# Optimization experiments

Measured on AMD Instinct MI355X. Metric: run time of the kernel, lower is better.

Reference implementation:

```python
import jax, jax.numpy as jnp
import numpy as np

NUM_HEADS = 4
TEMPERATURE = 1.0
EDGE_WEIGHT = 0.5


def setup_inputs() -> dict:
    key = jax.random.key(0)
    k1, k2, k3 = jax.random.split(key, 3)
    x = jax.random.normal(k1, (4, 2048, 512), dtype=jnp.float32)
    gate_w = jax.random.normal(k2, (1, 1), dtype=jnp.float32)
    gate_b = jax.random.normal(k3, (1,), dtype=jnp.float32)
    return {"x": x, "gate_w": gate_w, "gate_b": gate_b}


def _forward(x, gate_w, gate_b):
    B, N, C = x.shape
    H = NUM_HEADS
    hd = C // H
    # F.normalize(x, dim=-1) with eps=1e-12
    norm = jnp.linalg.norm(x, axis=-1, keepdims=True)
    x_norm = x / jnp.maximum(norm, 1e-12)
    # multi-head cosine-sim attention
    xh = x_norm.reshape(B, N, H, hd).transpose(0, 2, 1, 3)  # (B,H,N,hd)
    sim = jnp.einsum("bhnd,bhmd->bhnm", xh, xh) / (hd ** 0.5 * TEMPERATURE)
    attn = jax.nn.softmax(sim, axis=-1)
    xv = x.reshape(B, N, H, hd).transpose(0, 2, 1, 3)  # (B,H,N,hd)
    x_refined = jnp.einsum("bhnm,bhmd->bhnd", attn, xv)
    x_refined = x_refined.transpose(0, 2, 1, 3).reshape(B, N, C)
    # edge-variance mask (no_grad in torch -> stop_gradient)
    diff = jnp.var(x, axis=-1, keepdims=True, ddof=1)  # (B,N,1), unbiased like torch
    edge_mask = jax.nn.sigmoid((diff - diff.mean()) / (jnp.std(diff, ddof=1) + 1e-6))
    edge_mask = jax.lax.stop_gradient(edge_mask)
    x_refined = (1.0 + EDGE_WEIGHT * edge_mask) * x_refined
    # scalar gate: Linear(1,1) + Sigmoid on global mean
    gate_input = x.mean(axis=1, keepdims=True).mean(axis=-1, keepdims=True)  # (B,1,1)
    gate = jax.nn.sigmoid(gate_input * gate_w[0, 0] + gate_b[0])
    x_refined = gate * x_refined
    return x + x_refined


def reference(x, gate_w, gate_b):
    return _forward(x, gate_w, gate_b)
```

## Files before the change

kernel.cpp:

```cpp
#include <hip/hip_runtime.h>
#include <stdint.h>

#define B_   4
#define N_   2048
#define C_   512
#define H_   4
#define HD_  128
#define BN_  (B_ * N_)
#define NIT_ 32
#define SCALE_ 0.08838834764831845f

typedef __attribute__((ext_vector_type(8))) short  short8;
typedef __attribute__((ext_vector_type(4))) unsigned short ushort4_t;
typedef __attribute__((ext_vector_type(4))) float  float4_t;
typedef __attribute__((ext_vector_type(8))) __bf16 bf16x8;

static __device__ __forceinline__ unsigned short f2bf(float f) {
  union { float f; uint32_t u; } v; v.f = f;
  uint32_t r = v.u + 0x7FFFu + ((v.u >> 16) & 1u);
  return (unsigned short)(r >> 16);
}

static __device__ __forceinline__ float4_t mfma16(short8 a, short8 b, float4_t c) {
  return __builtin_amdgcn_mfma_f32_16x16x32_bf16(
      __builtin_bit_cast(bf16x8, a), __builtin_bit_cast(bf16x8, b), c, 0, 0, 0);
}

#define GLOAD16(SRC, DST)                                               \
  __builtin_amdgcn_global_load_lds(                                     \
      (const __attribute__((address_space(1))) void*)(SRC),             \
      (__attribute__((address_space(3))) void*)(DST), 16, 0, 0)

__global__ __launch_bounds__(256) void k_stats(
    const float* __restrict__ x, unsigned short* __restrict__ xnq,
    float* __restrict__ diff, float* __restrict__ toksum) {
  int tok  = blockIdx.x * 4 + (threadIdx.x >> 6);
  int lane = threadIdx.x & 63;
  const float* xr = x + (size_t)tok * C_;
  float4_t a = *(const float4_t*)(xr + lane * 8);
  float4_t b = *(const float4_t*)(xr + lane * 8 + 4);
  float s = 0.f, ss = 0.f;
#pragma unroll
  for (int j = 0; j < 4; ++j) {
    s  += a[j] + b[j];
    ss += a[j] * a[j] + b[j] * b[j];
  }
#pragma unroll
  for (int o = 1; o < 64; o <<= 1) {
    s  += __shfl_xor(s, o);
    ss += __shfl_xor(ss, o);
  }
  float rn = 1.f / fmaxf(sqrtf(ss), 1e-12f);
  short8 o8;
#pragma unroll
  for (int j = 0; j < 4; ++j) {
    o8[j]     = (short)f2bf(a[j] * rn);
    o8[j + 4] = (short)f2bf(b[j] * rn);
  }
  *(short8*)(xnq + (size_t)tok * C_ + lane * 8) = o8;
  if (lane == 0) {
    diff[tok]   = (ss - s * s * (1.f / C_)) * (1.f / (C_ - 1));
    toksum[tok] = s;
  }
}

__global__ __launch_bounds__(256) void k_transpose(
    const float* __restrict__ x, unsigned short* __restrict__ xvT) {
  __shared__ float tr[HD_][65];
  int bh = blockIdx.x & 15, nt = blockIdx.x >> 4;
  int b = bh >> 2, h = bh & 3;
  int n0 = nt * 64, c0 = h * HD_;
  int t = threadIdx.x;
  int dm = (t & 31) * 4;
  int nr = t >> 5;
#pragma unroll
  for (int p = 0; p < 8; ++p) {
    int n = p * 8 + nr;
    float4_t v = *(const float4_t*)(x + ((size_t)(b * N_ + n0 + n)) * C_ + c0 + dm);
#pragma unroll
    for (int k = 0; k < 4; ++k) tr[dm + k][n] = v[k];
  }
  __syncthreads();
#pragma unroll
  for (int p = 0; p < 4; ++p) {
    int c = p * 256 + t;
    int d = c >> 3, nc = (c & 7) * 8;
    short8 o8;
#pragma unroll
    for (int e = 0; e < 8; ++e) o8[e] = (short)f2bf(tr[d][nc + e]);
    *(short8*)(xvT + ((size_t)bh * HD_ + d) * N_ + n0 + nc) = o8;
  }
}

__global__ __launch_bounds__(256) void k_finalize(
    const float* __restrict__ diff, const float* __restrict__ toksum,
    const float* __restrict__ gw, const float* __restrict__ gb,
    float* __restrict__ stats) {
  __shared__ float sh[4][8];
  int t = threadIdx.x, l = t & 63, w = t >> 6;
  float s1 = 0.f, s2 = 0.f;
  for (int i = t; i < BN_; i += 256) { float d = diff[i]; s1 += d; s2 += d * d; }
  float bs0 = 0.f, bs1 = 0.f, bs2 = 0.f, bs3 = 0.f;
  for (int i = t; i < N_; i += 256) {
    bs0 += toksum[i];          bs1 += toksum[N_ + i];
    bs2 += toksum[2 * N_ + i]; bs3 += toksum[3 * N_ + i];
  }
#pragma unroll
  for (int o = 1; o < 64; o <<= 1) {
    s1 += __shfl_xor(s1, o);  s2 += __shfl_xor(s2, o);
    bs0 += __shfl_xor(bs0, o); bs1 += __shfl_xor(bs1, o);
    bs2 += __shfl_xor(bs2, o); bs3 += __shfl_xor(bs3, o);
  }
  if (l == 0) {
    sh[w][0] = s1; sh[w][1] = s2;
    sh[w][2] = bs0; sh[w][3] = bs1; sh[w][4] = bs2; sh[w][5] = bs3;
  }
  __syncthreads();
  if (t == 0) {
    float S1 = sh[0][0] + sh[1][0] + sh[2][0] + sh[3][0];
    float S2 = sh[0][1] + sh[1][1] + sh[2][1] + sh[3][1];
    float mean = S1 / (float)BN_;
    float var  = (S2 - S1 * S1 / (float)BN_) / (float)(BN_ - 1);
    float rstd = 1.f / (sqrtf(var) + 1e-6f);
    stats[0] = mean; stats[1] = rstd;
    float w00 = gw[0], bb = gb[0];
#pragma unroll
    for (int q = 0; q < 4; ++q) {
      float bsum = sh[0][2 + q] + sh[1][2 + q] + sh[2][2 + q] + sh[3][2 + q];
      float gi = bsum / (float)(N_ * C_);
      stats[2 + q] = 1.f / (1.f + __expf(-(gi * w00 + bb)));
    }
  }
}

__global__ __launch_bounds__(128) void k_attn(
    const float* __restrict__ x, const unsigned short* __restrict__ xnq,
    const unsigned short* __restrict__ xvT, const float* __restrict__ diff,
    const float* __restrict__ stats, float* __restrict__ out) {
  __shared__ unsigned short sm[32768];
  int i  = blockIdx.x;
  int bh = ((i & 7) << 1) | ((i >> 3) & 1);
  int qt = i >> 4;
  int b = bh >> 2, h = bh & 3, c0 = h * HD_;
  int tid = threadIdx.x, w = tid >> 6, l = tid & 63;
  int g = l >> 4, r = l & 15;
  int q0 = qt * 64 + w * 32;

  short8 qf[2][4];
  const unsigned short* qbase = xnq + ((size_t)(b * N_ + q0)) * C_ + c0;
#pragma unroll
  for (int sub = 0; sub < 2; ++sub)
#pragma unroll
    for (int cs = 0; cs < 4; ++cs)
      qf[sub][cs] = *(const short8*)(qbase + (size_t)(sub * 16 + r) * C_ + g * 8 + cs * 32);

  float4_t acc[2][8];
  float ls[2] = {0.f, 0.f};
#pragma unroll
  for (int sub = 0; sub < 2; ++sub)
#pragma unroll
    for (int dt = 0; dt < 8; ++dt)
      acc[sub][dt] = (float4_t){0.f, 0.f, 0.f, 0.f};

  auto stage = [&](int it, int cb) {
    const unsigned short* ks = xnq + ((size_t)(b * N_ + it * 64)) * C_ + c0;
    unsigned short* kd = &sm[cb * 8192];
#pragma unroll
    for (int jj = 0; jj < 8; ++jj) {
      int j = w * 8 + jj;
      int row = 4 * j + g;
      int ssl = r ^ (row & 15);
      GLOAD16(ks + (size_t)row * C_ + ssl * 8, kd + j * 512);
    }
    const unsigned short* vs = xvT + ((size_t)bh * HD_) * N_ + it * 64;
    unsigned short* vd = &sm[16384 + cb * 8192];
#pragma unroll
    for (int jj = 0; jj < 8; ++jj) {
      int j = w * 8 + jj;
      int d = 8 * j + (l >> 3);
      int ssl = (l & 7) ^ (d & 7);
      GLOAD16(vs + (size_t)d * N_ + ssl * 8, vd + j * 512);
    }
  };

  stage(0, 0);
  __syncthreads();

  for (int it = 0; it < NIT_; ++it) {
    int cb = it & 1;
    if (it + 1 < NIT_) stage(it + 1, cb ^ 1);
    const unsigned short* K = &sm[cb * 8192];
    const unsigned short* V = &sm[16384 + cb * 8192];

    float4_t p[2][4];
#pragma unroll
    for (int sub = 0; sub < 2; ++sub)
#pragma unroll
      for (int t4 = 0; t4 < 4; ++t4)
        p[sub][t4] = (float4_t){0.f, 0.f, 0.f, 0.f};

#pragma unroll
    for (int t4 = 0; t4 < 4; ++t4) {
#pragma unroll
      for (int cs = 0; cs < 4; ++cs) {
        short8 kf = *(const short8*)(K + (size_t)(t4 * 16 + r) * 128 +
                                     ((g * 8 + cs * 32) ^ (r * 8)));
        p[0][t4] = mfma16(kf, qf[0][cs], p[0][t4]);
        p[1][t4] = mfma16(kf, qf[1][cs], p[1][t4]);
      }
    }

    short8 pf[2][2];
#pragma unroll
    for (int sub = 0; sub < 2; ++sub)
#pragma unroll
      for (int t4 = 0; t4 < 4; ++t4) {
        float e0 = __expf(p[sub][t4][0] * SCALE_);
        float e1 = __expf(p[sub][t4][1] * SCALE_);
        float e2 = __expf(p[sub][t4][2] * SCALE_);
        float e3 = __expf(p[sub][t4][3] * SCALE_);
        ls[sub] += (e0 + e1) + (e2 + e3);
        pf[sub][t4 >> 1][(t4 & 1) * 4 + 0] = (short)f2bf(e0);
        pf[sub][t4 >> 1][(t4 & 1) * 4 + 1] = (short)f2bf(e1);
        pf[sub][t4 >> 1][(t4 & 1) * 4 + 2] = (short)f2bf(e2);
        pf[sub][t4 >> 1][(t4 & 1) * 4 + 3] = (short)f2bf(e3);
      }

    int sw = (r & 7) * 8;
#pragma unroll
    for (int dt = 0; dt < 8; ++dt) {
      const unsigned short* vrow = V + (size_t)(dt * 16 + r) * 64;
      union { short8 s8; ushort4_t h[2]; } vf0, vf1;
      vf0.h[0] = *(const ushort4_t*)(vrow + ((g * 4)      ^ sw));
      vf0.h[1] = *(const ushort4_t*)(vrow + ((g * 4 + 16) ^ sw));
      vf1.h[0] = *(const ushort4_t*)(vrow + ((g * 4 + 32) ^ sw));
      vf1.h[1] = *(const ushort4_t*)(vrow + ((g * 4 + 48) ^ sw));
      acc[0][dt] = mfma16(vf0.s8, pf[0][0], acc[0][dt]);
      acc[0][dt] = mfma16(vf1.s8, pf[0][1], acc[0][dt]);
      acc[1][dt] = mfma16(vf0.s8, pf[1][0], acc[1][dt]);
      acc[1][dt] = mfma16(vf1.s8, pf[1][1], acc[1][dt]);
    }
    __syncthreads();
  }

#pragma unroll
  for (int sub = 0; sub < 2; ++sub) {
    ls[sub] += __shfl_xor(ls[sub], 16);
    ls[sub] += __shfl_xor(ls[sub], 32);
  }
  float mean = stats[0], rstd = stats[1], gate = stats[2 + b];
#pragma unroll
  for (int sub = 0; sub < 2; ++sub) {
    int q = q0 + sub * 16 + r;
    float dv = diff[b * N_ + q];
    float em = 1.f / (1.f + __expf(-(dv - mean) * rstd));
    float f  = gate * (1.f + 0.5f * em) / ls[sub];
    const float* xr = x + ((size_t)(b * N_ + q)) * C_;
    float* orow = out + ((size_t)(b * N_ + q)) * C_;
#pragma unroll
    for (int dt = 0; dt < 8; ++dt) {
      int dcol = c0 + dt * 16 + g * 4;
      float4_t xin = *(const float4_t*)(xr + dcol);
      float4_t o;
#pragma unroll
      for (int j = 0; j < 4; ++j) o[j] = xin[j] + f * acc[sub][dt][j];
      *(float4_t*)(orow + dcol) = o;
    }
  }
}

extern "C" void kernel_launch(void* const* d_in, const int* in_sizes, int n_in,
                              void* d_out, int out_size, void* d_ws, size_t ws_size,
                              hipStream_t stream) {
  (void)in_sizes; (void)n_in; (void)out_size; (void)ws_size;
  const float* x  = (const float*)d_in[0];
  const float* gw = (const float*)d_in[1];
  const float* gb = (const float*)d_in[2];
  float* out = (float*)d_out;
  unsigned short* xnq = (unsigned short*)d_ws;
  unsigned short* xvT = xnq + (size_t)BN_ * C_;
  float* diff   = (float*)(xvT + (size_t)BN_ * C_);
  float* toksum = diff + BN_;
  float* stats  = toksum + BN_;
  hipLaunchKernelGGL(k_stats, dim3(BN_ / 4), dim3(256), 0, stream, x, xnq, diff, toksum);
  hipLaunchKernelGGL(k_transpose, dim3(512), dim3(256), 0, stream, x, xvT);
  hipLaunchKernelGGL(k_finalize, dim3(1), dim3(256), 0, stream, diff, toksum, gw, gb, stats);
  hipLaunchKernelGGL(k_attn, dim3(512), dim3(128), 0, stream, x, xnq, xvT, diff, stats, out);
}
```

Baseline: 80.79 us.

## Split attention work over four waves per block with pre-swizzled V and packed bf16 conversion

The attention kernel now launches 256 threads per block, with each wave owning 16 query rows instead of 32. This halves per-wave accumulator registers and spreads the K/V staging loads across four waves. The V swizzle moves into the transpose kernel's global write layout, so staging becomes a plain copy. Softmax uses exp2 with a folded log2e scale and the v_cvt_pk_bf16_f32 packed conversion, and s_setprio brackets are placed around the MFMA sections. The trade-off is that each K/V tile loaded into LDS now feeds fewer MFMAs per wave, which lowers LDS reuse per wave.

```diff
diff --git a/kernel.cpp b/kernel.cpp
--- a/kernel.cpp
+++ b/kernel.cpp
@@ -8,7 +8,7 @@
 #define HD_  128
 #define BN_  (B_ * N_)
 #define NIT_ 32
-#define SCALE_ 0.08838834764831845f
+#define SCALE_LOG2E 0.1275129727595311f
 
 typedef __attribute__((ext_vector_type(8))) short  short8;
 typedef __attribute__((ext_vector_type(4))) unsigned short ushort4_t;
@@ -20,6 +20,18 @@
   uint32_t r = v.u + 0x7FFFu + ((v.u >> 16) & 1u);
   return (unsigned short)(r >> 16);
 }
+
+static __device__ __forceinline__ uint32_t cvtpk_bf16(float lo, float hi) {
+  uint32_t r;
+  asm("v_cvt_pk_bf16_f32 %0, %1, %2" : "=v"(r) : "v"(lo), "v"(hi));
+  return r;
+}
+
+#if __has_builtin(__builtin_amdgcn_exp2f)
+#define EXP2(x) __builtin_amdgcn_exp2f(x)
+#else
+#define EXP2(x) exp2f(x)
+#endif
 
 static __device__ __forceinline__ float4_t mfma16(short8 a, short8 b, float4_t c) {
   return __builtin_amdgcn_mfma_f32_16x16x32_bf16(
@@ -85,10 +97,17 @@
   for (int p = 0; p < 4; ++p) {
     int c = p * 256 + t;
     int d = c >> 3, nc = (c & 7) * 8;
-    short8 o8;
-#pragma unroll
-    for (int e = 0; e < 8; ++e) o8[e] = (short)f2bf(tr[d][nc + e]);
-    *(short8*)(xvT + ((size_t)bh * HD_ + d) * N_ + n0 + nc) = o8;
+    int P = ((d & 7) << 1) | ((d >> 3) & 1);
+    int q0h = nc >> 2;
+    ushort4_t h0, h1;
+#pragma unroll
+    for (int e = 0; e < 4; ++e) {
+      h0[e] = f2bf(tr[d][nc + e]);
+      h1[e] = f2bf(tr[d][nc + 4 + e]);
+    }
+    unsigned short* base = xvT + ((size_t)bh * HD_ + d) * N_ + n0;
+    *(ushort4_t*)(base + (((q0h    ) ^ P) << 2)) = h0;
+    *(ushort4_t*)(base + (((q0h + 1) ^ P) << 2)) = h1;
   }
 }
 
@@ -133,7 +152,7 @@
   }
 }
 
-__global__ __launch_bounds__(128) void k_attn(
+__global__ __launch_bounds__(256) void k_attn(
     const float* __restrict__ x, const unsigned short* __restrict__ xnq,
     const unsigned short* __restrict__ xvT, const float* __restrict__ diff,
     const float* __restrict__ stats, float* __restrict__ out) {
@@ -144,30 +163,26 @@
   int b = bh >> 2, h = bh & 3, c0 = h * HD_;
   int tid = threadIdx.x, w = tid >> 6, l = tid & 63;
   int g = l >> 4, r = l & 15;
-  int q0 = qt * 64 + w * 32;
-
-  short8 qf[2][4];
+  int r3 = (r >> 3) & 1;
+  int q0 = qt * 64 + w * 16;
+
+  short8 qf[4];
   const unsigned short* qbase = xnq + ((size_t)(b * N_ + q0)) * C_ + c0;
 #pragma unroll
-  for (int sub = 0; sub < 2; ++sub)
-#pragma unroll
-    for (int cs = 0; cs < 4; ++cs)
-      qf[sub][cs] = *(const short8*)(qbase + (size_t)(sub * 16 + r) * C_ + g * 8 + cs * 32);
-
-  float4_t acc[2][8];
-  float ls[2] = {0.f, 0.f};
-#pragma unroll
-  for (int sub = 0; sub < 2; ++sub)
-#pragma unroll
-    for (int dt = 0; dt < 8; ++dt)
-      acc[sub][dt] = (float4_t){0.f, 0.f, 0.f, 0.f};
+  for (int cs = 0; cs < 4; ++cs)
+    qf[cs] = *(const short8*)(qbase + (size_t)r * C_ + g * 8 + cs * 32);
+
+  float4_t acc[8];
+  float ls = 0.f;
+#pragma unroll
+  for (int dt = 0; dt < 8; ++dt) acc[dt] = (float4_t){0.f, 0.f, 0.f, 0.f};
 
   auto stage = [&](int it, int cb) {
     const unsigned short* ks = xnq + ((size_t)(b * N_ + it * 64)) * C_ + c0;
     unsigned short* kd = &sm[cb * 8192];
 #pragma unroll
-    for (int jj = 0; jj < 8; ++jj) {
-      int j = w * 8 + jj;
+    for (int jj = 0; jj < 4; ++jj) {
+      int j = w * 4 + jj;
       int row = 4 * j + g;
       int ssl = r ^ (row & 15);
       GLOAD16(ks + (size_t)row * C_ + ssl * 8, kd + j * 512);
@@ -175,11 +190,10 @@
     const unsigned short* vs = xvT + ((size_t)bh * HD_) * N_ + it * 64;
     unsigned short* vd = &sm[16384 + cb * 8192];
 #pragma unroll
-    for (int jj = 0; jj < 8; ++jj) {
-      int j = w * 8 + jj;
+    for (int jj = 0; jj < 4; ++jj) {
+      int j = w * 4 + jj;
       int d = 8 * j + (l >> 3);
-      int ssl = (l & 7) ^ (d & 7);
-      GLOAD16(vs + (size_t)d * N_ + ssl * 8, vd + j * 512);
+      GLOAD16(vs + (size_t)d * N_ + (l & 7) * 8, vd + j * 512);
     }
   };
 
@@ -192,80 +206,68 @@
     const unsigned short* K = &sm[cb * 8192];
     const unsigned short* V = &sm[16384 + cb * 8192];
 
-    float4_t p[2][4];
-#pragma unroll
-    for (int sub = 0; sub < 2; ++sub)
-#pragma unroll
-      for (int t4 = 0; t4 < 4; ++t4)
-        p[sub][t4] = (float4_t){0.f, 0.f, 0.f, 0.f};
-
+    float4_t p[4];
+#pragma unroll
+    for (int t4 = 0; t4 < 4; ++t4) p[t4] = (float4_t){0.f, 0.f, 0.f, 0.f};
+
+    __builtin_amdgcn_s_setprio(1);
 #pragma unroll
     for (int t4 = 0; t4 < 4; ++t4) {
 #pragma unroll
       for (int cs = 0; cs < 4; ++cs) {
         short8 kf = *(const short8*)(K + (size_t)(t4 * 16 + r) * 128 +
                                      ((g * 8 + cs * 32) ^ (r * 8)));
-        p[0][t4] = mfma16(kf, qf[0][cs], p[0][t4]);
-        p[1][t4] = mfma16(kf, qf[1][cs], p[1][t4]);
+        p[t4] = mfma16(kf, qf[cs], p[t4]);
       }
     }
-
-    short8 pf[2][2];
-#pragma unroll
-    for (int sub = 0; sub < 2; ++sub)
-#pragma unroll
-      for (int t4 = 0; t4 < 4; ++t4) {
-        float e0 = __expf(p[sub][t4][0] * SCALE_);
-        float e1 = __expf(p[sub][t4][1] * SCALE_);
-        float e2 = __expf(p[sub][t4][2] * SCALE_);
-        float e3 = __expf(p[sub][t4][3] * SCALE_);
-        ls[sub] += (e0 + e1) + (e2 + e3);
-        pf[sub][t4 >> 1][(t4 & 1) * 4 + 0] = (short)f2bf(e0);
-        pf[sub][t4 >> 1][(t4 & 1) * 4 + 1] = (short)f2bf(e1);
-        pf[sub][t4 >> 1][(t4 & 1) * 4 + 2] = (short)f2bf(e2);
-        pf[sub][t4 >> 1][(t4 & 1) * 4 + 3] = (short)f2bf(e3);
-      }
-
-    int sw = (r & 7) * 8;
+    __builtin_amdgcn_s_setprio(0);
+
+    union { short8 s8; uint32_t u[4]; } pf[2];
+#pragma unroll
+    for (int t4 = 0; t4 < 4; ++t4) {
+      float e0 = EXP2(p[t4][0] * SCALE_LOG2E);
+      float e1 = EXP2(p[t4][1] * SCALE_LOG2E);
+      float e2 = EXP2(p[t4][2] * SCALE_LOG2E);
+      float e3 = EXP2(p[t4][3] * SCALE_LOG2E);
+      ls += (e0 + e1) + (e2 + e3);
+      pf[t4 >> 1].u[(t4 & 1) * 2 + 0] = cvtpk_bf16(e0, e1);
+      pf[t4 >> 1].u[(t4 & 1) * 2 + 1] = cvtpk_bf16(e2, e3);
+    }
+
+    int X = ((r & 7) << 3) | (r3 << 2);
+    __builtin_amdgcn_s_setprio(1);
 #pragma unroll
     for (int dt = 0; dt < 8; ++dt) {
       const unsigned short* vrow = V + (size_t)(dt * 16 + r) * 64;
       union { short8 s8; ushort4_t h[2]; } vf0, vf1;
-      vf0.h[0] = *(const ushort4_t*)(vrow + ((g * 4)      ^ sw));
-      vf0.h[1] = *(const ushort4_t*)(vrow + ((g * 4 + 16) ^ sw));
-      vf1.h[0] = *(const ushort4_t*)(vrow + ((g * 4 + 32) ^ sw));
-      vf1.h[1] = *(const ushort4_t*)(vrow + ((g * 4 + 48) ^ sw));
-      acc[0][dt] = mfma16(vf0.s8, pf[0][0], acc[0][dt]);
-      acc[0][dt] = mfma16(vf1.s8, pf[0][1], acc[0][dt]);
-      acc[1][dt] = mfma16(vf0.s8, pf[1][0], acc[1][dt]);
-      acc[1][dt] = mfma16(vf1.s8, pf[1][1], acc[1][dt]);
-    }
+      vf0.h[0] = *(const ushort4_t*)(vrow + ((g * 4)      ^ X));
+      vf0.h[1] = *(const ushort4_t*)(vrow + ((g * 4 + 16) ^ X));
+      vf1.h[0] = *(const ushort4_t*)(vrow + ((g * 4 + 32) ^ X));
+      vf1.h[1] = *(const ushort4_t*)(vrow + ((g * 4 + 48) ^ X));
+      acc[dt] = mfma16(vf0.s8, pf[0].s8, acc[dt]);
+      acc[dt] = mfma16(vf1.s8, pf[1].s8, acc[dt]);
+    }
+    __builtin_amdgcn_s_setprio(0);
     __syncthreads();
   }
 
-#pragma unroll
-  for (int sub = 0; sub < 2; ++sub) {
-    ls[sub] += __shfl_xor(ls[sub], 16);
-    ls[sub] += __shfl_xor(ls[sub], 32);
-  }
+  ls += __shfl_xor(ls, 16);
+  ls += __shfl_xor(ls, 32);
   float mean = stats[0], rstd = stats[1], gate = stats[2 + b];
-#pragma unroll
-  for (int sub = 0; sub < 2; ++sub) {
-    int q = q0 + sub * 16 + r;
-    float dv = diff[b * N_ + q];
-    float em = 1.f / (1.f + __expf(-(dv - mean) * rstd));
-    float f  = gate * (1.f + 0.5f * em) / ls[sub];
-    const float* xr = x + ((size_t)(b * N_ + q)) * C_;
-    float* orow = out + ((size_t)(b * N_ + q)) * C_;
-#pragma unroll
-    for (int dt = 0; dt < 8; ++dt) {
-      int dcol = c0 + dt * 16 + g * 4;
-      float4_t xin = *(const float4_t*)(xr + dcol);
-      float4_t o;
-#pragma unroll
-      for (int j = 0; j < 4; ++j) o[j] = xin[j] + f * acc[sub][dt][j];
-      *(float4_t*)(orow + dcol) = o;
-    }
+  int q = q0 + r;
+  float dv = diff[b * N_ + q];
+  float em = 1.f / (1.f + __expf(-(dv - mean) * rstd));
+  float f  = gate * (1.f + 0.5f * em) / ls;
+  const float* xr = x + ((size_t)(b * N_ + q)) * C_;
+  float* orow = out + ((size_t)(b * N_ + q)) * C_;
+#pragma unroll
+  for (int dt = 0; dt < 8; ++dt) {
+    int dcol = c0 + dt * 16 + g * 4;
+    float4_t xin = *(const float4_t*)(xr + dcol);
+    float4_t o;
+#pragma unroll
+    for (int j = 0; j < 4; ++j) o[j] = xin[j] + f * acc[dt][j];
+    *(float4_t*)(orow + dcol) = o;
   }
 }
 
@@ -285,5 +287,5 @@
   hipLaunchKernelGGL(k_stats, dim3(BN_ / 4), dim3(256), 0, stream, x, xnq, diff, toksum);
   hipLaunchKernelGGL(k_transpose, dim3(512), dim3(256), 0, stream, x, xvT);
   hipLaunchKernelGGL(k_finalize, dim3(1), dim3(256), 0, stream, diff, toksum, gw, gb, stats);
-  hipLaunchKernelGGL(k_attn, dim3(512), dim3(128), 0, stream, x, xnq, xvT, diff, stats, out);
-}
+  hipLaunchKernelGGL(k_attn, dim3(512), dim3(256), 0, stream, x, xnq, xvT, diff, stats, out);
+}
```

New measurement: 77.43 us. -4.2%, faster.
